# Optimization experiments

Measured on AMD Instinct MI355X. Metric: run time of the kernel, lower is better.

## Reference

```python
import jax, jax.numpy as jnp
import numpy as np


def setup_inputs() -> dict:
    key = jax.random.key(0)
    kq, kk, kv = jax.random.split(key, 3)
    B, S, D = 4, 4096, 64
    q = jax.random.normal(kq, (B, S, D), dtype=jnp.float32)
    k = jax.random.normal(kk, (B, S, D), dtype=jnp.float32)
    v = jax.random.normal(kv, (B, S, D), dtype=jnp.float32)
    return {"q": q, "k": k, "v": v}


def reference(q, k, v):
    # Faithful math of the original blocked loop:
    #   output_i += exp(Q_i @ K_j^T) @ V_j, summed over all column blocks j
    # which is exactly unnormalized exponential attention:
    #   out = exp(Q K^T) V  (no 1/sqrt(d) scaling, no softmax normalization,
    #   no max-subtraction -- matching the source module's math).
    scores = jnp.einsum("bqd,bkd->bqk", q, k)  # [B, Sq, Sk]
    return jnp.einsum("bqk,bkd->bqd", jnp.exp(scores), v)  # [B, Sq, D]
```

## Files before the change

### kernel.cpp

```cpp
#include <hip/hip_runtime.h>
#include <hip/hip_bf16.h>


typedef short    s16x4 __attribute__((ext_vector_type(4)));
typedef short    s16x8 __attribute__((ext_vector_type(8)));
typedef _Float16 h16x8 __attribute__((ext_vector_type(8)));
typedef float    fx4   __attribute__((ext_vector_type(4)));
typedef float    fx16  __attribute__((ext_vector_type(16)));

constexpr int S = 4096, D = 64, BQ = 64, BN = 128;
constexpr int TILES = S / BN;
constexpr int HALF_TILES = TILES / 2;
constexpr int TILE_SHORTS  = 16 * 512;
constexpr int BATCH_SHORTS = TILES * TILE_SHORTS;

__device__ __forceinline__ unsigned short f2bf(float x) {
    unsigned u = __float_as_uint(x);
    u = (u + 0x7FFFu + ((u >> 16) & 1u)) >> 16;
    return (unsigned short)u;
}
__device__ __forceinline__ float bf2f(unsigned short h) {
    return __uint_as_float(((unsigned)h) << 16);
}
__device__ __forceinline__ unsigned short f2h(float x) {
    union { _Float16 h; unsigned short s; } u;
    u.h = (_Float16)x;
    return u.s;
}
__device__ __forceinline__ unsigned pack_bf16(float lo, float hi) {
    __hip_bfloat162 r = __float22bfloat162_rn(make_float2(lo, hi));
    union { __hip_bfloat162 b; unsigned u; } c;
    c.b = r;
    return c.u;
}

__global__ __launch_bounds__(256) void prep2(
    const float* __restrict__ k, const float* __restrict__ v,
    unsigned short* __restrict__ kf, unsigned short* __restrict__ vf)
{
    __shared__ unsigned short tile[128 * 72];
    const int tid   = threadIdx.x;
    const int which = blockIdx.x & 1;
    const int t     = (blockIdx.x >> 1) & 31;
    const int b     = blockIdx.x >> 6;
    const float* src = (which ? v : k) + ((size_t)b * S + t * BN) * D;

    #pragma unroll
    for (int i = 0; i < 8; ++i) {
        int f   = i * 256 + tid;
        int row = f >> 4;
        int c4  = (f & 15) << 2;
        float4 x = *(const float4*)(src + row * D + c4);
        s16x4 o;
        if (which) o = (s16x4){(short)f2bf(x.x), (short)f2bf(x.y),
                               (short)f2bf(x.z), (short)f2bf(x.w)};
        else       o = (s16x4){(short)f2h(x.x), (short)f2h(x.y),
                               (short)f2h(x.z), (short)f2h(x.w)};
        *(s16x4*)&tile[row * 72 + c4] = o;
    }
    __syncthreads();

    const int lane = tid & 63;
    unsigned short* dst = (which ? vf : kf) + (size_t)b * BATCH_SHORTS + t * TILE_SHORTS;
    #pragma unroll
    for (int i = 0; i < 4; ++i) {
        int c = (tid >> 6) * 4 + i;
        s16x8 o;
        if (which == 0) {
            int row = (c >> 2) * 32 + (lane & 31);
            int dc  = (c & 3) * 16 + (lane >> 5) * 8;
            o = *(const s16x8*)&tile[row * 72 + dc];
        } else {
            int r0 = (c >> 1) * 16 + (lane >> 5) * 8;
            int dc = (c & 1) * 32 + (lane & 31);
            #pragma unroll
            for (int j = 0; j < 8; ++j) o[j] = (short)tile[(r0 + j) * 72 + dc];
        }
        *(s16x8*)(dst + c * 512 + lane * 8) = o;
    }
}

__global__ __launch_bounds__(512, 4) void attn_main3(
    const float* __restrict__ q, const unsigned short* __restrict__ kf,
    const unsigned short* __restrict__ vf, float* __restrict__ partial)
{
    __shared__ unsigned short smem[2 * 2 * TILE_SHORTS];

    const int tid = threadIdx.x, lane = tid & 63, w = tid >> 6;
    const int h = lane >> 5, m5 = lane & 31;
    const int mt = w & 1, kkq = w >> 1;
    const int b = blockIdx.y, q0 = blockIdx.x * BQ;
    const int kh = blockIdx.z;
    const int t0 = kh * HALF_TILES;

    const unsigned short* kfb = kf + (size_t)b * BATCH_SHORTS;
    const unsigned short* vfb = vf + (size_t)b * BATCH_SHORTS;

    h16x8 qf[4];
    {
        const float* qrow = q + ((size_t)b * S + q0 + mt * 32 + m5) * D + h * 8;
        #pragma unroll
        for (int ks = 0; ks < 4; ++ks) {
            float4 a = *(const float4*)(qrow + ks * 16);
            float4 c = *(const float4*)(qrow + ks * 16 + 4);
            qf[ks] = (h16x8){(_Float16)a.x, (_Float16)a.y, (_Float16)a.z, (_Float16)a.w,
                             (_Float16)c.x, (_Float16)c.y, (_Float16)c.z, (_Float16)c.w};
        }
    }

    fx16 oacc[2] = {};

    auto issue = [&](int t, int bi) {
        unsigned short* base = &smem[bi * 2 * TILE_SHORTS];
        #pragma unroll
        for (int ii = 0; ii < 4; ++ii) {
            int c = (ii & 1) * 8 + w;
            const unsigned short* g = (ii < 2 ? kfb : vfb)
                + (size_t)t * TILE_SHORTS + c * 512 + lane * 8;
            unsigned short* l = base + (ii < 2 ? 0 : TILE_SHORTS) + c * 512 + lane * 8;
            __builtin_amdgcn_global_load_lds(
                (const __attribute__((address_space(1))) unsigned int*)g,
                (__attribute__((address_space(3))) unsigned int*)l, 16, 0, 0);
        }
    };

    issue(t0, 0);

    for (int i = 0; i < HALF_TILES; ++i) {
        const int bi = i & 1;
        __asm__ volatile("" ::: "memory");
        __builtin_amdgcn_s_waitcnt(0x0F70);
        __builtin_amdgcn_s_barrier();
        __asm__ volatile("" ::: "memory");
        if (i + 1 < HALF_TILES) issue(t0 + i + 1, bi ^ 1);

        const unsigned short* kb = &smem[bi * 2 * TILE_SHORTS];
        const unsigned short* vb = kb + TILE_SHORTS;

        fx16 sa = {};
        #pragma unroll
        for (int ks = 0; ks < 4; ++ks) {
            h16x8 a = *(const h16x8*)(kb + (kkq * 4 + ks) * 512 + lane * 8);
            sa = __builtin_amdgcn_mfma_f32_32x32x16_f16(a, qf[ks], sa, 0, 0, 0);
        }

        unsigned p01[8], sw[8];
        #pragma unroll
        for (int r = 0; r < 8; ++r)
            p01[r] = pack_bf16(__expf(sa[2 * r]), __expf(sa[2 * r + 1]));
        #pragma unroll
        for (int r = 0; r < 8; ++r) sw[r] = (unsigned)__shfl_xor((int)p01[r], 32, 64);

        union { unsigned u[4]; s16x8 v; } A1u, A2u;
        A1u.u[0] = h ? sw[2]  : p01[0];  A1u.u[1] = h ? sw[3]  : p01[1];
        A1u.u[2] = h ? p01[2] : sw[0];   A1u.u[3] = h ? p01[3] : sw[1];
        A2u.u[0] = h ? sw[6]  : p01[4];  A2u.u[1] = h ? sw[7]  : p01[5];
        A2u.u[2] = h ? p01[6] : sw[4];   A2u.u[3] = h ? p01[7] : sw[5];

        #pragma unroll
        for (int u = 0; u < 2; ++u) {
            s16x8 Au = u ? A2u.v : A1u.v;
            int ss = kkq * 2 + u;
            #pragma unroll
            for (int dt = 0; dt < 2; ++dt) {
                s16x8 vv = *(const s16x8*)(vb + (ss * 2 + dt) * 512 + lane * 8);
                oacc[dt] = __builtin_amdgcn_mfma_f32_32x32x16_bf16(Au, vv, oacc[dt], 0, 0, 0);
            }
        }
    }

    __syncthreads();
    float* scratch = (float*)smem;
    if (kkq > 0) {
        float* dst = scratch + (size_t)(mt * 3 + (kkq - 1)) * 2048;
        #pragma unroll
        for (int dt = 0; dt < 2; ++dt)
            #pragma unroll
            for (int r = 0; r < 16; ++r)
                dst[(dt * 16 + r) * 64 + lane] = oacc[dt][r];
    }
    __syncthreads();
    if (kkq == 0) {
        float* pout = partial + ((size_t)kh * gridDim.y + b) * S * D;
        #pragma unroll
        for (int dt = 0; dt < 2; ++dt)
            #pragma unroll
            for (int r = 0; r < 16; ++r) {
                float val = oacc[dt][r];
                #pragma unroll
                for (int p = 0; p < 3; ++p)
                    val += scratch[(size_t)(mt * 3 + p) * 2048 + (dt * 16 + r) * 64 + lane];
                int row = q0 + mt * 32 + (r & 3) + 8 * (r >> 2) + 4 * h;
                pout[(size_t)row * D + dt * 32 + m5] = val;
            }
    }
}

__global__ __launch_bounds__(256) void reduce_out(
    const float4* __restrict__ p0, const float4* __restrict__ p1,
    float4* __restrict__ o, int n4)
{
    int i = blockIdx.x * 256 + threadIdx.x;
    if (i < n4) {
        float4 a = p0[i], b = p1[i];
        o[i] = make_float4(a.x + b.x, a.y + b.y, a.z + b.z, a.w + b.w);
    }
}

__global__ __launch_bounds__(1024) void attn_fallback(
    const float* __restrict__ q, const float* __restrict__ k,
    const float* __restrict__ v, float* __restrict__ out)
{
    __shared__ unsigned short Kh[64][72];
    __shared__ unsigned short Kl[64][72];
    __shared__ unsigned short Vt[64][68];
    __shared__ unsigned short Pf[64][72];

    const int tid = threadIdx.x, lane = tid & 63, wave = tid >> 6;
    const int quad = lane >> 4, tq = lane & 15;
    const int kkb = wave & 3, mba = wave >> 2;
    const int b = blockIdx.y, q0 = blockIdx.x * 64;
    const float* qb = q + (size_t)b * S * D;
    const float* kb = k + (size_t)b * S * D;
    const float* vb = v + (size_t)b * S * D;
    float* ob = out + (size_t)b * S * D;

    s16x8 qh[2], ql[2];
    {
        const float* qrow = qb + (size_t)(q0 + mba * 16 + tq) * D;
        #pragma unroll
        for (int ks = 0; ks < 2; ++ks) {
            const float* src = qrow + ks * 32 + quad * 8;
            float4 f0 = *(const float4*)src;
            float4 f1 = *(const float4*)(src + 4);
            float f[8] = {f0.x, f0.y, f0.z, f0.w, f1.x, f1.y, f1.z, f1.w};
            #pragma unroll
            for (int j = 0; j < 8; ++j) {
                unsigned short hh = f2bf(f[j]);
                qh[ks][j] = (short)hh;
                ql[ks][j] = (short)f2bf(f[j] - bf2f(hh));
            }
        }
    }
    fx4 oacc = {0.f, 0.f, 0.f, 0.f};
    const int krow = tid >> 4, kc4 = (tid & 15) << 2;
    const int vd = tid & 63, vk = (tid >> 6) << 2;

    for (int t = 0; t < S / 64; ++t) {
        __syncthreads();
        const float* kt = kb + (size_t)(t * 64 + krow) * D;
        const float* vt = vb + (size_t)(t * 64 + vk) * D;
        {
            float4 kv = *(const float4*)(kt + kc4);
            unsigned short h0 = f2bf(kv.x), h1 = f2bf(kv.y), h2 = f2bf(kv.z), h3 = f2bf(kv.w);
            s16x4 a = {(short)h0, (short)h1, (short)h2, (short)h3};
            s16x4 l4 = {(short)f2bf(kv.x - bf2f(h0)), (short)f2bf(kv.y - bf2f(h1)),
                        (short)f2bf(kv.z - bf2f(h2)), (short)f2bf(kv.w - bf2f(h3))};
            *(s16x4*)&Kh[krow][kc4] = a;
            *(s16x4*)&Kl[krow][kc4] = l4;
            const float* vs = vt + vd;
            s16x4 vv = {(short)f2bf(vs[0]), (short)f2bf(vs[D]),
                        (short)f2bf(vs[2 * D]), (short)f2bf(vs[3 * D])};
            *(s16x4*)&Vt[vd][vk] = vv;
        }
        __syncthreads();
        fx4 sacc = {0.f, 0.f, 0.f, 0.f};
        #pragma unroll
        for (int ks = 0; ks < 2; ++ks) {
            s16x8 kah = *(const s16x8*)&Kh[kkb * 16 + tq][ks * 32 + quad * 8];
            s16x8 kal = *(const s16x8*)&Kl[kkb * 16 + tq][ks * 32 + quad * 8];
            sacc = __builtin_amdgcn_mfma_f32_16x16x32_bf16(kah, qh[ks], sacc, 0, 0, 0);
            sacc = __builtin_amdgcn_mfma_f32_16x16x32_bf16(kah, ql[ks], sacc, 0, 0, 0);
            sacc = __builtin_amdgcn_mfma_f32_16x16x32_bf16(kal, qh[ks], sacc, 0, 0, 0);
        }
        s16x4 pp = {(short)f2bf(__expf(sacc[0])), (short)f2bf(__expf(sacc[1])),
                    (short)f2bf(__expf(sacc[2])), (short)f2bf(__expf(sacc[3]))};
        *(s16x4*)&Pf[mba * 16 + tq][kkb * 16 + (quad << 2)] = pp;
        __syncthreads();
        #pragma unroll
        for (int ks = 0; ks < 2; ++ks) {
            s16x8 pa = *(const s16x8*)&Pf[mba * 16 + tq][ks * 32 + quad * 8];
            const unsigned short* vr = &Vt[kkb * 16 + tq][ks * 32 + quad * 8];
            s16x4 va = *(const s16x4*)vr;
            s16x4 vb2 = *(const s16x4*)(vr + 4);
            s16x8 vfull = __builtin_shufflevector(va, vb2, 0, 1, 2, 3, 4, 5, 6, 7);
            oacc = __builtin_amdgcn_mfma_f32_16x16x32_bf16(pa, vfull, oacc, 0, 0, 0);
        }
    }
    #pragma unroll
    for (int r = 0; r < 4; ++r)
        ob[(size_t)(q0 + mba * 16 + quad * 4 + r) * D + kkb * 16 + tq] = oacc[r];
}

extern "C" void kernel_launch(void* const* d_in, const int* in_sizes, int n_in,
                              void* d_out, int out_size, void* d_ws, size_t ws_size,
                              hipStream_t stream) {
    const float* q = (const float*)d_in[0];
    const float* k = (const float*)d_in[1];
    const float* v = (const float*)d_in[2];
    float* out = (float*)d_out;
    const int nbatch = in_sizes[0] / (S * D);
    const size_t elems = (size_t)nbatch * S * D;

    const size_t need = elems * 2 * 2 + elems * 2 * 4;
    if (nbatch == 4 && ws_size >= need && d_ws != nullptr) {
        unsigned short* kf = (unsigned short*)d_ws;
        unsigned short* vf = kf + elems;
        float* partial = (float*)(vf + elems);

        prep2<<<nbatch * TILES * 2, 256, 0, stream>>>(k, v, kf, vf);
        dim3 grid(S / BQ, nbatch, 2);
        attn_main3<<<grid, 512, 0, stream>>>(q, kf, vf, partial);
        const int n4 = (int)(elems / 4);
        reduce_out<<<(n4 + 255) / 256, 256, 0, stream>>>(
            (const float4*)partial, (const float4*)(partial + elems),
            (float4*)out, n4);
    } else {
        dim3 grid(S / 64, nbatch);
        attn_fallback<<<grid, 1024, 0, stream>>>(q, k, v, out);
    }
}
```

Measured before the change: 96.99 us.

## Double query rows per block to reuse K/V tiles, use exp2 and permlane swap

```diff
diff --git a/kernel.cpp b/kernel.cpp
--- a/kernel.cpp
+++ b/kernel.cpp
@@ -8,7 +8,8 @@
 typedef float    fx4   __attribute__((ext_vector_type(4)));
 typedef float    fx16  __attribute__((ext_vector_type(16)));
 
-constexpr int S = 4096, D = 64, BQ = 64, BN = 128;
+constexpr int S = 4096, D = 64, BN = 128;
+constexpr int QROWS = 128;
 constexpr int TILES = S / BN;
 constexpr int HALF_TILES = TILES / 2;
 constexpr int TILE_SHORTS  = 16 * 512;
@@ -32,6 +33,13 @@
     union { __hip_bfloat162 b; unsigned u; } c;
     c.b = r;
     return c.u;
+}
+__device__ __forceinline__ float ex2(float x) {
+#if __has_builtin(__builtin_amdgcn_exp2f)
+    return __builtin_amdgcn_exp2f(x);
+#else
+    return exp2f(x);
+#endif
 }
 
 __global__ __launch_bounds__(256) void prep2(
@@ -80,7 +88,7 @@
     }
 }
 
-__global__ __launch_bounds__(512, 4) void attn_main3(
+__global__ __launch_bounds__(512, 2) void attn_main4(
     const float* __restrict__ q, const unsigned short* __restrict__ kf,
     const unsigned short* __restrict__ vf, float* __restrict__ partial)
 {
@@ -88,27 +96,32 @@
 
     const int tid = threadIdx.x, lane = tid & 63, w = tid >> 6;
     const int h = lane >> 5, m5 = lane & 31;
-    const int mt = w & 1, kkq = w >> 1;
-    const int b = blockIdx.y, q0 = blockIdx.x * BQ;
+    const int mh = w & 1, kkq = w >> 1;
+    const int b = blockIdx.y, q0 = blockIdx.x * QROWS;
     const int kh = blockIdx.z;
     const int t0 = kh * HALF_TILES;
 
     const unsigned short* kfb = kf + (size_t)b * BATCH_SHORTS;
     const unsigned short* vfb = vf + (size_t)b * BATCH_SHORTS;
 
-    h16x8 qf[4];
-    {
-        const float* qrow = q + ((size_t)b * S + q0 + mt * 32 + m5) * D + h * 8;
+    const float LOG2E = 1.4426950408889634f;
+    h16x8 qf[2][4];
+    #pragma unroll
+    for (int mt = 0; mt < 2; ++mt) {
+        const float* qrow = q + ((size_t)b * S + q0 + mh * 64 + mt * 32 + m5) * D + h * 8;
         #pragma unroll
         for (int ks = 0; ks < 4; ++ks) {
             float4 a = *(const float4*)(qrow + ks * 16);
             float4 c = *(const float4*)(qrow + ks * 16 + 4);
-            qf[ks] = (h16x8){(_Float16)a.x, (_Float16)a.y, (_Float16)a.z, (_Float16)a.w,
-                             (_Float16)c.x, (_Float16)c.y, (_Float16)c.z, (_Float16)c.w};
-        }
-    }
-
-    fx16 oacc[2] = {};
+            qf[mt][ks] = (h16x8){
+                (_Float16)(a.x * LOG2E), (_Float16)(a.y * LOG2E),
+                (_Float16)(a.z * LOG2E), (_Float16)(a.w * LOG2E),
+                (_Float16)(c.x * LOG2E), (_Float16)(c.y * LOG2E),
+                (_Float16)(c.z * LOG2E), (_Float16)(c.w * LOG2E)};
+        }
+    }
+
+    fx16 oacc[2][2] = {};
 
     auto issue = [&](int t, int bi) {
         unsigned short* base = &smem[bi * 2 * TILE_SHORTS];
@@ -137,62 +150,94 @@
         const unsigned short* kb = &smem[bi * 2 * TILE_SHORTS];
         const unsigned short* vb = kb + TILE_SHORTS;
 
-        fx16 sa = {};
+        fx16 sa[2] = {};
         #pragma unroll
         for (int ks = 0; ks < 4; ++ks) {
             h16x8 a = *(const h16x8*)(kb + (kkq * 4 + ks) * 512 + lane * 8);
-            sa = __builtin_amdgcn_mfma_f32_32x32x16_f16(a, qf[ks], sa, 0, 0, 0);
-        }
-
-        unsigned p01[8], sw[8];
-        #pragma unroll
-        for (int r = 0; r < 8; ++r)
-            p01[r] = pack_bf16(__expf(sa[2 * r]), __expf(sa[2 * r + 1]));
-        #pragma unroll
-        for (int r = 0; r < 8; ++r) sw[r] = (unsigned)__shfl_xor((int)p01[r], 32, 64);
-
-        union { unsigned u[4]; s16x8 v; } A1u, A2u;
-        A1u.u[0] = h ? sw[2]  : p01[0];  A1u.u[1] = h ? sw[3]  : p01[1];
-        A1u.u[2] = h ? p01[2] : sw[0];   A1u.u[3] = h ? p01[3] : sw[1];
-        A2u.u[0] = h ? sw[6]  : p01[4];  A2u.u[1] = h ? sw[7]  : p01[5];
-        A2u.u[2] = h ? p01[6] : sw[4];   A2u.u[3] = h ? p01[7] : sw[5];
+            #pragma unroll
+            for (int mt = 0; mt < 2; ++mt)
+                sa[mt] = __builtin_amdgcn_mfma_f32_32x32x16_f16(a, qf[mt][ks], sa[mt], 0, 0, 0);
+        }
+
+        unsigned p01[2][8];
+        #pragma unroll
+        for (int mt = 0; mt < 2; ++mt)
+            #pragma unroll
+            for (int rp = 0; rp < 8; ++rp)
+                p01[mt][rp] = pack_bf16(ex2(sa[mt][2 * rp]), ex2(sa[mt][2 * rp + 1]));
+
+        union frag { unsigned u[4]; s16x8 v; };
+        frag A[2][2];
+        #pragma unroll
+        for (int mt = 0; mt < 2; ++mt) {
+#if __has_builtin(__builtin_amdgcn_permlane32_swap)
+            typedef unsigned uix2 __attribute__((ext_vector_type(2)));
+            uix2 r0 = __builtin_amdgcn_permlane32_swap(p01[mt][0], p01[mt][2], false, false);
+            uix2 r1 = __builtin_amdgcn_permlane32_swap(p01[mt][1], p01[mt][3], false, false);
+            A[mt][0].u[0] = r0.x; A[mt][0].u[1] = r1.x;
+            A[mt][0].u[2] = r0.y; A[mt][0].u[3] = r1.y;
+            uix2 r2 = __builtin_amdgcn_permlane32_swap(p01[mt][4], p01[mt][6], false, false);
+            uix2 r3 = __builtin_amdgcn_permlane32_swap(p01[mt][5], p01[mt][7], false, false);
+            A[mt][1].u[0] = r2.x; A[mt][1].u[1] = r3.x;
+            A[mt][1].u[2] = r2.y; A[mt][1].u[3] = r3.y;
+#else
+            unsigned sw[8];
+            #pragma unroll
+            for (int rp = 0; rp < 8; ++rp)
+                sw[rp] = (unsigned)__shfl_xor((int)p01[mt][rp], 32, 64);
+            A[mt][0].u[0] = h ? sw[2]        : p01[mt][0];
+            A[mt][0].u[1] = h ? sw[3]        : p01[mt][1];
+            A[mt][0].u[2] = h ? p01[mt][2]   : sw[0];
+            A[mt][0].u[3] = h ? p01[mt][3]   : sw[1];
+            A[mt][1].u[0] = h ? sw[6]        : p01[mt][4];
+            A[mt][1].u[1] = h ? sw[7]        : p01[mt][5];
+            A[mt][1].u[2] = h ? p01[mt][6]   : sw[4];
+            A[mt][1].u[3] = h ? p01[mt][7]   : sw[5];
+#endif
+        }
 
         #pragma unroll
         for (int u = 0; u < 2; ++u) {
-            s16x8 Au = u ? A2u.v : A1u.v;
             int ss = kkq * 2 + u;
             #pragma unroll
             for (int dt = 0; dt < 2; ++dt) {
                 s16x8 vv = *(const s16x8*)(vb + (ss * 2 + dt) * 512 + lane * 8);
-                oacc[dt] = __builtin_amdgcn_mfma_f32_32x32x16_bf16(Au, vv, oacc[dt], 0, 0, 0);
+                #pragma unroll
+                for (int mt = 0; mt < 2; ++mt)
+                    oacc[mt][dt] = __builtin_amdgcn_mfma_f32_32x32x16_bf16(
+                        A[mt][u].v, vv, oacc[mt][dt], 0, 0, 0);
             }
         }
     }
 
     __syncthreads();
     float* scratch = (float*)smem;
-    if (kkq > 0) {
-        float* dst = scratch + (size_t)(mt * 3 + (kkq - 1)) * 2048;
-        #pragma unroll
-        for (int dt = 0; dt < 2; ++dt)
-            #pragma unroll
-            for (int r = 0; r < 16; ++r)
-                dst[(dt * 16 + r) * 64 + lane] = oacc[dt][r];
-    }
-    __syncthreads();
-    if (kkq == 0) {
-        float* pout = partial + ((size_t)kh * gridDim.y + b) * S * D;
-        #pragma unroll
-        for (int dt = 0; dt < 2; ++dt)
-            #pragma unroll
-            for (int r = 0; r < 16; ++r) {
-                float val = oacc[dt][r];
+    float* pout = partial + ((size_t)kh * gridDim.y + b) * S * D;
+    #pragma unroll
+    for (int dt = 0; dt < 2; ++dt) {
+        if (kkq > 0) {
+            float* dst = scratch + (size_t)(mh * 3 + (kkq - 1)) * 2048;
+            #pragma unroll
+            for (int mt = 0; mt < 2; ++mt)
                 #pragma unroll
-                for (int p = 0; p < 3; ++p)
-                    val += scratch[(size_t)(mt * 3 + p) * 2048 + (dt * 16 + r) * 64 + lane];
-                int row = q0 + mt * 32 + (r & 3) + 8 * (r >> 2) + 4 * h;
-                pout[(size_t)row * D + dt * 32 + m5] = val;
-            }
+                for (int r = 0; r < 16; ++r)
+                    dst[(mt * 16 + r) * 64 + lane] = oacc[mt][dt][r];
+        }
+        __syncthreads();
+        if (kkq == 0) {
+            #pragma unroll
+            for (int mt = 0; mt < 2; ++mt)
+                #pragma unroll
+                for (int r = 0; r < 16; ++r) {
+                    float val = oacc[mt][dt][r];
+                    #pragma unroll
+                    for (int p = 0; p < 3; ++p)
+                        val += scratch[(size_t)(mh * 3 + p) * 2048 + (mt * 16 + r) * 64 + lane];
+                    int row = q0 + mh * 64 + mt * 32 + (r & 3) + 8 * (r >> 2) + 4 * h;
+                    pout[(size_t)row * D + dt * 32 + m5] = val;
+                }
+        }
+        __syncthreads();
     }
 }
 
@@ -309,8 +354,8 @@
         float* partial = (float*)(vf + elems);
 
         prep2<<<nbatch * TILES * 2, 256, 0, stream>>>(k, v, kf, vf);
-        dim3 grid(S / BQ, nbatch, 2);
-        attn_main3<<<grid, 512, 0, stream>>>(q, kf, vf, partial);
+        dim3 grid(S / QROWS, nbatch, 2);
+        attn_main4<<<grid, 512, 0, stream>>>(q, kf, vf, partial);
         const int n4 = (int)(elems / 4);
         reduce_out<<<(n4 + 255) / 256, 256, 0, stream>>>(
             (const float4*)partial, (const float4*)(partial + elems),
```

Measured after the change: 91.94 us. 1.05x faster.
